# Kernel tuning notes

Hardware: AMD Instinct MI355X
Metric: run time of the kernel (lower is better)

## Reference

```python
import jax, jax.numpy as jnp
import numpy as np

UNITS = 300
MDN_MIXES = 8  # Config.mdn_mixes: 3*8=24 MDN params + 1 length = 25-dim feedback
FEAT = 25
GATE_IN = 2 * FEAT  # concat(inputs, prev_output)


def setup_inputs() -> dict:
    key = jax.random.key(0)
    ks = jax.random.split(key, 12)
    B, T = 2048, 512
    x = jax.random.uniform(ks[0], (B, T, FEAT), dtype=jnp.float32)
    s = 0.05
    kernel = jax.random.normal(ks[1], (FEAT, 4 * UNITS), dtype=jnp.float32) * s
    recurrent_kernel = jax.random.normal(ks[2], (UNITS, 4 * UNITS), dtype=jnp.float32) * s
    # unit_forget_bias: zeros except forget-gate slice = ones
    bias = jnp.concatenate([
        jnp.zeros((UNITS,), jnp.float32),
        jnp.ones((UNITS,), jnp.float32),
        jnp.zeros((2 * UNITS,), jnp.float32),
    ])
    # MLPGate: 2-layer MLP combining the two 25-dim distributions -> 24-dim
    mlp_w1 = jax.random.normal(ks[3], (GATE_IN, GATE_IN), dtype=jnp.float32) * s
    mlp_b1 = jnp.zeros((GATE_IN,), jnp.float32)
    mlp_w2 = jax.random.normal(ks[4], (GATE_IN, FEAT - 1), dtype=jnp.float32) * s
    mlp_b2 = jnp.zeros((FEAT - 1,), jnp.float32)
    # MDN heads on h (units -> mdn_mixes each)
    wa = jax.random.normal(ks[5], (UNITS, MDN_MIXES), dtype=jnp.float32) * s
    ba = jnp.zeros((MDN_MIXES,), jnp.float32)
    wm = jax.random.normal(ks[6], (UNITS, MDN_MIXES), dtype=jnp.float32) * s
    bm = jnp.zeros((MDN_MIXES,), jnp.float32)
    ws = jax.random.normal(ks[7], (UNITS, MDN_MIXES), dtype=jnp.float32) * s
    bs = jnp.zeros((MDN_MIXES,), jnp.float32)
    return {
        'x': x, 'kernel': kernel, 'recurrent_kernel': recurrent_kernel, 'bias': bias,
        'mlp_w1': mlp_w1, 'mlp_b1': mlp_b1, 'mlp_w2': mlp_w2, 'mlp_b2': mlp_b2,
        'wa': wa, 'ba': ba, 'wm': wm, 'bm': bm, 'ws': ws, 'bs': bs,
    }


def _hard_sigmoid(z):
    return jnp.clip(0.2 * z + 0.5, 0.0, 1.0)


def _nnelu(z):
    return 1.0 + jax.nn.elu(z)


def reference(x, kernel, recurrent_kernel, bias,
              mlp_w1, mlp_b1, mlp_w2, mlp_b2,
              wa, ba, wm, bm, ws, bs):
    B = x.shape[0]
    dt = x.dtype

    def step(carry, xt):
        h, c, prev = carry  # [B,U], [B,U], [B,25]
        il = xt[:, 24:25]
        pl = prev[:, 24:25]
        combined = il + pl
        denom = jnp.maximum(combined, jnp.asarray(1e-8, dt))  # LengthNormalizer
        inp2 = jnp.concatenate([xt[:, :24], il / denom], axis=1)
        prev2 = jnp.concatenate([prev[:, :24], pl / denom], axis=1)
        # MLP gate combining the two distributions
        g = jax.nn.relu(jnp.concatenate([inp2, prev2], axis=1) @ mlp_w1 + mlp_b1)
        g = g @ mlp_w2 + mlp_b2  # [B,24]
        gate_out = jnp.concatenate([g, combined], axis=1)  # [B,25]
        # LSTM gates (split-kernel math == fused without dropout)
        z = gate_out @ kernel + h @ recurrent_kernel + bias  # [B,4U]
        zi, zf, zc, zo = jnp.split(z, 4, axis=1)
        i = _hard_sigmoid(zi)
        f = _hard_sigmoid(zf)
        o = _hard_sigmoid(zo)
        c_new = f * c + i * jnp.tanh(zc)
        h_new = o * jnp.tanh(c_new)
        # MDN heads
        alpha = jax.nn.softmax(h_new @ wa + ba, axis=-1)
        mu = h_new @ wm + bm
        sigma = _nnelu(h_new @ ws + bs)
        mdn = jnp.concatenate([alpha, mu, sigma, combined], axis=1)  # [B,25]
        return (h_new, c_new, mdn), mdn

    h0 = jnp.zeros((B, UNITS), dt)
    c0 = jnp.zeros((B, UNITS), dt)
    prev0 = jnp.zeros((B, FEAT), dt)
    xt = jnp.swapaxes(x, 0, 1)  # [T,B,25]
    _, ys = jax.lax.scan(step, (h0, c0, prev0), xt)
    return jnp.swapaxes(ys, 0, 1)  # [B,T,25]
```

## Files before the change

kernel.cpp:

```cpp
#include <hip/hip_runtime.h>
#include <math.h>

#define BB 2048
#define TT 512
#define NFEAT 25
#define UNITS 300
#define RPB 16
#define NBLK (BB/RPB)
#define NT 512
#define NKS 11
#define TPW 10
#define AROW 360
#define F8ROW 352
#define GROW 72

#define OFF_B0 0
#define SZ_B0  (8*TPW*512)
#define OFF_M1 (OFF_B0 + SZ_B0)
#define SZ_M1  (4*2*512)
#define OFF_M2 (OFF_M1 + SZ_M1)
#define SZ_M2  (2*2*512)
#define OFF_H  (OFF_M2 + SZ_M2)
#define SZ_H   (2*NKS*512)
#define OFF_F8 (OFF_H + SZ_H)
#define SZ_F8B (8*100*512)
#define SW_SZ  (SZ_M1 + SZ_M2 + SZ_H)
#define SWM1   0
#define SWM2   (SZ_M1)
#define SWH    (SZ_M1 + SZ_M2)

typedef __attribute__((ext_vector_type(4))) float f32x4;
typedef __attribute__((ext_vector_type(8))) short bf16x8;

static __device__ __forceinline__ unsigned short f2bf(float f) {
    union { float f; unsigned u; } x; x.f = f;
    unsigned r = (x.u + 0x7fffu + ((x.u >> 16) & 1u)) >> 16;
    return (unsigned short)r;
}
static __device__ __forceinline__ unsigned char f2f8(float f) {
    return (unsigned char)(__builtin_amdgcn_cvt_pk_fp8_f32(f, 0.f, 0, false) & 0xff);
}
static __device__ __forceinline__ float ftanh(float v) {
    float e = __builtin_amdgcn_exp2f(v * 2.8853900817779268f);
    return 1.f - 2.f * __builtin_amdgcn_rcpf(e + 1.f);
}

static __device__ __forceinline__ int zcol(int c) { return (c & 3) * 300 + (c >> 2); }

__global__ __launch_bounds__(256) void conv_b0(
    const float* __restrict__ wk, unsigned short* __restrict__ dst)
{
    int idx = blockIdx.x * 256 + threadIdx.x;
    if (idx >= SZ_B0) return;
    int j = idx & 7, n = (idx >> 3) & 15, kg = (idx >> 7) & 3, q = idx >> 9;
    int i = q % TPW, w = q / TPW;
    int k = kg * 8 + j, c = (w + 8 * i) * 16 + n;
    float v = (k < 25 && c < 1200) ? wk[k * 1200 + zcol(c)] : 0.f;
    dst[OFF_B0 + idx] = f2bf(v);
}

__global__ __launch_bounds__(256) void conv_b8(
    const float* __restrict__ wr, unsigned char* __restrict__ dst8)
{
    int idx = blockIdx.x * 256 + threadIdx.x;
    if (idx >= SZ_F8B) return;
    int j = idx & 7, n = (idx >> 3) & 15, kg = (idx >> 7) & 3, q = idx >> 9;
    int i = q % TPW, ks1 = (q / TPW) % 10, w = q / 100;
    int k = (ks1 + 1) * 32 + kg * 8 + j, c = (w + 8 * i) * 16 + n;
    float v = (k >= 32 && k < 332 && c < 1200) ? wr[(k - 32) * 1200 + zcol(c)] : 0.f;
    dst8[idx] = f2f8(v);
}

__global__ __launch_bounds__(256) void conv_gen(
    const float* __restrict__ W, unsigned short* __restrict__ dst,
    int K, int N, int nks, int total)
{
    int idx = blockIdx.x * 256 + threadIdx.x;
    if (idx >= total) return;
    int j = idx & 7, n = (idx >> 3) & 15, kg = (idx >> 7) & 3, qq = idx >> 9;
    int ks = qq % nks, nt = qq / nks;
    int k = ks * 32 + kg * 8 + j, col = nt * 16 + n;
    float v = (k < K && col < N) ? W[k * N + col] : 0.f;
    dst[idx] = f2bf(v);
}

__global__ __launch_bounds__(256) void conv_heads(
    const float* __restrict__ wa, const float* __restrict__ wm,
    const float* __restrict__ wsg, unsigned short* __restrict__ dst)
{
    int idx = blockIdx.x * 256 + threadIdx.x;
    if (idx >= SZ_H) return;
    int j = idx & 7, n = (idx >> 3) & 15, kg = (idx >> 7) & 3, qq = idx >> 9;
    int ks = qq % NKS, nt = qq / NKS;
    int k = ks * 32 + kg * 8 + j, col = nt * 16 + n;
    float v = 0.f;
    if (k >= 32 && k < 332 && col < 24) {
        int u = k - 32, h = col >> 3, m = col & 7;
        const float* W = (h == 0) ? wa : (h == 1) ? wm : wsg;
        v = W[u * 8 + m];
    }
    dst[OFF_H + idx] = f2bf(v);
}

#define MFMA   __builtin_amdgcn_mfma_f32_16x16x32_bf16
#define MFMA8  __builtin_amdgcn_mfma_f32_16x16x32_fp8_fp8

__global__ __launch_bounds__(NT, 2)
void dilstm(
    const float* __restrict__ x,
    const unsigned short* __restrict__ wf,
    const float* __restrict__ bz,
    const float* __restrict__ b1v,
    const float* __restrict__ b2v,
    const float* __restrict__ ba,
    const float* __restrict__ bm,
    const float* __restrict__ bs,
    float* __restrict__ out)
{
    __shared__ unsigned short Abf[2][RPB][AROW];
    __shared__ __attribute__((aligned(16))) unsigned char Af8[2][RPB][F8ROW];
    __shared__ unsigned short Gbf[RPB][GROW];
    __shared__ unsigned short G1b[RPB][GROW];
    __shared__ float Sc[RPB][24];
    __shared__ float BzS[1280];
    __shared__ float B1S[64];
    __shared__ float B2S[32];
    __shared__ float Zw[8][2][16][20];
    __shared__ unsigned short SW[SW_SZ];

    const int t = threadIdx.x;
    const int lane = t & 63, wv = t >> 6;
    const int arow = lane & 15, akg = lane >> 4;
    const int crow0 = akg * 4;
    const int u_l = lane & 3, rr = lane >> 2;
    const int row0 = blockIdx.x * RPB;

    for (int i = t; i < 2 * RPB * AROW; i += NT) ((unsigned short*)Abf)[i] = 0;
    for (int i = t; i < 2 * RPB * F8ROW; i += NT) ((unsigned char*)Af8)[i] = 0;
    for (int i = t; i < RPB * GROW; i += NT) { ((unsigned short*)Gbf)[i] = 0; ((unsigned short*)G1b)[i] = 0; }
    for (int i = t; i < SW_SZ; i += NT) SW[i] = wf[OFF_M1 + i];
    for (int i = t; i < 1280; i += NT)
        BzS[i] = (i < 1200) ? bz[zcol(i)] : 0.f;
    if (t < 64) B1S[t] = (t < 50) ? b1v[t] : 0.f;
    else if (t < 96) B2S[t - 64] = (t - 64 < 24) ? b2v[t - 64] : 0.f;

    float hbias = 0.f;
    {
        int c1 = wv * 16 + arow;
        if (wv < 2 && c1 < 24)
            hbias = (c1 < 8) ? ba[c1] : (c1 < 16) ? bm[c1 - 8] : bs[c1 - 16];
    }

    float creg[TPW];
    #pragma unroll
    for (int i = 0; i < TPW; ++i) creg[i] = 0.f;

    const unsigned short* bw0 = wf + OFF_B0 + wv * (TPW * 512) + (lane << 3);
    const unsigned char*  bw8 = (const unsigned char*)(wf + OFF_F8) + (size_t)wv * (100 * 512) + (lane << 3);

    const int rA = t / 25, eA = t - (t / 25) * 25;
    float combreg = 0.f, xreg = 0.f;
    if (t < RPB * NFEAT) xreg = x[((size_t)(row0 + rA) * TT) * NFEAT + eA];
    __syncthreads();

    if (t < RPB * NFEAT) {
        if (eA < 24) {
            Gbf[rA][eA] = f2bf(xreg);
        } else {
            float comb = xreg;
            combreg = comb;
            float denom = fmaxf(comb, 1e-8f);
            Gbf[rA][24] = f2bf(xreg / denom);
            Abf[0][rA][24] = f2bf(comb);
        }
    }
    __syncthreads();

    for (int ts = 0; ts < TT; ++ts) {
        const int p = ts & 1;

        f32x4 acc[TPW];
        #pragma unroll
        for (int i = 0; i < TPW; ++i) acc[i] = (f32x4){0.f, 0.f, 0.f, 0.f};

        if (wv == 0) {
            bf16x8 ga0 = *(const bf16x8*)&Gbf[arow][akg * 8];
            bf16x8 ga1 = *(const bf16x8*)&Gbf[arow][32 + akg * 8];
            #pragma unroll
            for (int ct = 0; ct < 4; ++ct) {
                bf16x8 b0 = *(const bf16x8*)&SW[SWM1 + (ct * 2 + 0) * 512 + (lane << 3)];
                bf16x8 b1 = *(const bf16x8*)&SW[SWM1 + (ct * 2 + 1) * 512 + (lane << 3)];
                f32x4 a1c = {0.f, 0.f, 0.f, 0.f};
                a1c = MFMA(ga0, b0, a1c, 0, 0, 0);
                a1c = MFMA(ga1, b1, a1c, 0, 0, 0);
                int col = ct * 16 + arow;
                if (col < 50) {
                    #pragma unroll
                    for (int rg = 0; rg < 4; ++rg)
                        G1b[crow0 + rg][col] = f2bf(fmaxf(a1c[rg] + B1S[col], 0.f));
                }
            }
            bf16x8 ha0 = *(const bf16x8*)&G1b[arow][akg * 8];
            bf16x8 ha1 = *(const bf16x8*)&G1b[arow][32 + akg * 8];
            #pragma unroll
            for (int ct = 0; ct < 2; ++ct) {
                bf16x8 b0 = *(const bf16x8*)&SW[SWM2 + (ct * 2 + 0) * 512 + (lane << 3)];
                bf16x8 b1 = *(const bf16x8*)&SW[SWM2 + (ct * 2 + 1) * 512 + (lane << 3)];
                f32x4 a2c = {0.f, 0.f, 0.f, 0.f};
                a2c = MFMA(ha0, b0, a2c, 0, 0, 0);
                a2c = MFMA(ha1, b1, a2c, 0, 0, 0);
                int col = ct * 16 + arow;
                if (col < 24) {
                    #pragma unroll
                    for (int rg = 0; rg < 4; ++rg)
                        Abf[p][crow0 + rg][col] = f2bf(a2c[rg] + B2S[col]);
                }
            }
        }

        if (t < RPB * NFEAT && ts + 1 < TT)
            xreg = x[((size_t)(row0 + rA) * TT + (ts + 1)) * NFEAT + eA];

        {
            const unsigned char* af8p = &Af8[p][0][0] + arow * F8ROW + akg * 8;
            const unsigned char* bp = bw8;
            long long bbA[TPW], bbB[TPW];
            #pragma unroll
            for (int i = 0; i < TPW; ++i)
                bbA[i] = *(const long long*)(bp + i * 512);
            #pragma unroll 1
            for (int pr = 0; pr < 5; ++pr) {
                const int ks = 2 * pr + 1;
                #pragma unroll
                for (int i = 0; i < TPW; ++i)
                    bbB[i] = *(const long long*)(bp + 5120 + i * 512);
                long long a8a = *(const long long*)(af8p + ks * 32);
                #pragma unroll
                for (int i = 0; i < TPW; ++i)
                    acc[i] = MFMA8(a8a, bbA[i], acc[i], 0, 0, 0);
                if (pr < 4) {
                    #pragma unroll
                    for (int i = 0; i < TPW; ++i)
                        bbA[i] = *(const long long*)(bp + 10240 + i * 512);
                }
                long long a8b = *(const long long*)(af8p + ks * 32 + 32);
                #pragma unroll
                for (int i = 0; i < TPW; ++i)
                    acc[i] = MFMA8(a8b, bbB[i], acc[i], 0, 0, 0);
                bp += 10240;
            }
        }
        __syncthreads();

        {
            bf16x8 bb0[TPW];
            #pragma unroll
            for (int i = 0; i < TPW; ++i)
                bb0[i] = *(const bf16x8*)(bw0 + i * 512);
            bf16x8 aA = *(const bf16x8*)&Abf[p][arow][akg * 8];
            #pragma unroll
            for (int i = 0; i < TPW; ++i)
                acc[i] = MFMA(aA, bb0[i], acc[i], 0, 0, 0);

            *(f32x4*)&Zw[wv][0][arow][crow0] = acc[0];
            #pragma unroll
            for (int i = 0; i < TPW; ++i) {
                if (i + 1 < TPW)
                    *(f32x4*)&Zw[wv][(i + 1) & 1][arow][crow0] = acc[i + 1];
                f32x4 bz4 = *(const f32x4*)&BzS[(wv + 8 * i) * 16 + 4 * u_l];
                const float* zp = &Zw[wv][i & 1][4 * u_l][rr];
                float zi = zp[0]  + bz4[0];
                float zf = zp[20] + bz4[1];
                float zc = zp[40] + bz4[2];
                float zo = zp[60] + bz4[3];
                if (wv + 8 * i < 75) {
                    float ig = fminf(fmaxf(0.2f * zi + 0.5f, 0.f), 1.f);
                    float fg = fminf(fmaxf(0.2f * zf + 0.5f, 0.f), 1.f);
                    float og = fminf(fmaxf(0.2f * zo + 0.5f, 0.f), 1.f);
                    float cn = fg * creg[i] + ig * ftanh(zc);
                    creg[i] = cn;
                    float hn = og * ftanh(cn);
                    int hc = 32 + (wv + 8 * i) * 4 + u_l;
                    Abf[p ^ 1][rr][hc] = f2bf(hn);
                    Af8[p ^ 1][rr][hc] = f2f8(hn);
                }
            }
        }
        __syncthreads();

        if (wv < 2) {
            f32x4 acc3 = {0.f, 0.f, 0.f, 0.f};
            #pragma unroll
            for (int ks = 1; ks < NKS; ++ks) {
                bf16x8 a = *(const bf16x8*)&Abf[p ^ 1][arow][ks * 32 + akg * 8];
                bf16x8 b = *(const bf16x8*)&SW[SWH + (wv * NKS + ks) * 512 + (lane << 3)];
                acc3 = MFMA(a, b, acc3, 0, 0, 0);
            }
            int col = wv * 16 + arow;
            if (col < 24) {
                #pragma unroll
                for (int rg = 0; rg < 4; ++rg)
                    Sc[crow0 + rg][col] = acc3[rg] + hbias;
            }
        }
        __syncthreads();

        if (t < RPB * NFEAT) {
            float v;
            if (eA < 8) {
                float mx = Sc[rA][0];
                #pragma unroll
                for (int m = 1; m < 8; ++m) mx = fmaxf(mx, Sc[rA][m]);
                float sum = 0.f;
                #pragma unroll
                for (int m = 0; m < 8; ++m)
                    sum += __builtin_amdgcn_exp2f((Sc[rA][m] - mx) * 1.4426950408889634f);
                v = __builtin_amdgcn_exp2f((Sc[rA][eA] - mx) * 1.4426950408889634f) / sum;
            } else if (eA < 16) {
                v = Sc[rA][eA];
            } else if (eA < 24) {
                float s = Sc[rA][eA];
                v = (s > 0.f) ? (1.f + s) : __builtin_amdgcn_exp2f(s * 1.4426950408889634f);
            } else {
                v = combreg;
            }
            out[((size_t)(row0 + rA) * TT + ts) * NFEAT + eA] = v;
            if (eA < 24) {
                Gbf[rA][eA]      = f2bf(xreg);
                Gbf[rA][25 + eA] = f2bf(v);
            } else {
                float comb = xreg + combreg;
                float denom = fmaxf(comb, 1e-8f);
                Gbf[rA][24] = f2bf(xreg / denom);
                Gbf[rA][49] = f2bf(combreg / denom);
                Abf[p ^ 1][rA][24] = f2bf(comb);
                combreg = comb;
            }
        }
        __syncthreads();
    }
}

extern "C" void kernel_launch(void* const* d_in, const int* in_sizes, int n_in,
                              void* d_out, int out_size, void* d_ws, size_t ws_size,
                              hipStream_t stream) {
    const float* x   = (const float*)d_in[0];
    const float* wk  = (const float*)d_in[1];
    const float* wr  = (const float*)d_in[2];
    const float* bz  = (const float*)d_in[3];
    const float* w1  = (const float*)d_in[4];
    const float* b1  = (const float*)d_in[5];
    const float* w2  = (const float*)d_in[6];
    const float* b2  = (const float*)d_in[7];
    const float* wa  = (const float*)d_in[8];
    const float* ba  = (const float*)d_in[9];
    const float* wm  = (const float*)d_in[10];
    const float* bm  = (const float*)d_in[11];
    const float* wsg = (const float*)d_in[12];
    const float* bs  = (const float*)d_in[13];
    float* out = (float*)d_out;
    unsigned short* wf = (unsigned short*)d_ws;
    unsigned char*  wf8 = (unsigned char*)(wf + OFF_F8);

    conv_b0<<<(SZ_B0 + 255) / 256, 256, 0, stream>>>(wk, wf);
    conv_b8<<<(SZ_F8B + 255) / 256, 256, 0, stream>>>(wr, wf8);
    conv_gen<<<(SZ_M1 + 255) / 256, 256, 0, stream>>>(w1, wf + OFF_M1, 50, 50, 2, SZ_M1);
    conv_gen<<<(SZ_M2 + 255) / 256, 256, 0, stream>>>(w2, wf + OFF_M2, 50, 24, 2, SZ_M2);
    conv_heads<<<(SZ_H + 255) / 256, 256, 0, stream>>>(wa, wm, wsg, wf);
    dilstm<<<NBLK, NT, 0, stream>>>(x, wf, bz, b1, b2, ba, bm, bs, out);
}
```

Before: 4.139 ms.

## Fold MLP second layer into LSTM input kernel and drop double-buffered A tiles

Precomputes w2 @ kernel[:24] as a fused fp8 weight block, so the MLP's second layer and the input-kernel bf16 MFMA collapse into two extra fp8 k-slices of the recurrent GEMM. The combined-length column becomes a scalar times a row of kernel, added in fp32, and b2 is folded into the bias. The first MLP layer is spread over 4 waves instead of 1. The Abf/Af8 tiles are no longer double-buffered. This shortens the serial per-step chain and removes a bf16 GEMM pass, at the cost of fp8 precision on the fused weights and the MLP activations (scaled by 0.125 to fit the fp8 range).

```diff
diff --git a/kernel.cpp b/kernel.cpp
--- a/kernel.cpp
+++ b/kernel.cpp
@@ -8,29 +8,28 @@
 #define RPB 16
 #define NBLK (BB/RPB)
 #define NT 512
+#define KS12 12
 #define NKS 11
 #define TPW 10
-#define AROW 360
-#define F8ROW 352
+#define HROW 360
+#define F8ROW 392
 #define GROW 72
 
-#define OFF_B0 0
-#define SZ_B0  (8*TPW*512)
-#define OFF_M1 (OFF_B0 + SZ_B0)
+#define OFF_M1 0
 #define SZ_M1  (4*2*512)
-#define OFF_M2 (OFF_M1 + SZ_M1)
-#define SZ_M2  (2*2*512)
-#define OFF_H  (OFF_M2 + SZ_M2)
+#define OFF_H  (OFF_M1 + SZ_M1)
 #define SZ_H   (2*NKS*512)
-#define OFF_F8 (OFF_H + SZ_H)
-#define SZ_F8B (8*100*512)
-#define SW_SZ  (SZ_M1 + SZ_M2 + SZ_H)
+#define OFF_BZ (OFF_H + SZ_H)
+#define OFF_WK (OFF_BZ + 2560)
+#define OFF_F8 (OFF_WK + 2560)
+#define SZ_F8B (8*KS12*TPW*512)
+#define SW_SZ  (SZ_M1 + SZ_H)
 #define SWM1   0
-#define SWM2   (SZ_M1)
-#define SWH    (SZ_M1 + SZ_M2)
+#define SWH    (SZ_M1)
 
 typedef __attribute__((ext_vector_type(4))) float f32x4;
 typedef __attribute__((ext_vector_type(8))) short bf16x8;
+typedef long long ll8;
 
 static __device__ __forceinline__ unsigned short f2bf(float f) {
     union { float f; unsigned u; } x; x.f = f;
@@ -44,31 +43,51 @@
     float e = __builtin_amdgcn_exp2f(v * 2.8853900817779268f);
     return 1.f - 2.f * __builtin_amdgcn_rcpf(e + 1.f);
 }
-
 static __device__ __forceinline__ int zcol(int c) { return (c & 3) * 300 + (c >> 2); }
 
-__global__ __launch_bounds__(256) void conv_b0(
-    const float* __restrict__ wk, unsigned short* __restrict__ dst)
-{
-    int idx = blockIdx.x * 256 + threadIdx.x;
-    if (idx >= SZ_B0) return;
-    int j = idx & 7, n = (idx >> 3) & 15, kg = (idx >> 7) & 3, q = idx >> 9;
-    int i = q % TPW, w = q / TPW;
-    int k = kg * 8 + j, c = (w + 8 * i) * 16 + n;
-    float v = (k < 25 && c < 1200) ? wk[k * 1200 + zcol(c)] : 0.f;
-    dst[OFF_B0 + idx] = f2bf(v);
-}
-
 __global__ __launch_bounds__(256) void conv_b8(
-    const float* __restrict__ wr, unsigned char* __restrict__ dst8)
+    const float* __restrict__ wk, const float* __restrict__ wr,
+    const float* __restrict__ w2, unsigned char* __restrict__ dst8)
 {
     int idx = blockIdx.x * 256 + threadIdx.x;
     if (idx >= SZ_F8B) return;
     int j = idx & 7, n = (idx >> 3) & 15, kg = (idx >> 7) & 3, q = idx >> 9;
-    int i = q % TPW, ks1 = (q / TPW) % 10, w = q / 100;
-    int k = (ks1 + 1) * 32 + kg * 8 + j, c = (w + 8 * i) * 16 + n;
-    float v = (k >= 32 && k < 332 && c < 1200) ? wr[(k - 32) * 1200 + zcol(c)] : 0.f;
+    int i = q % TPW, ks = (q / TPW) % KS12, w = q / (TPW * KS12);
+    int k = ks * 32 + kg * 8 + j, c = (w + 8 * i) * 16 + n;
+    float v = 0.f;
+    if (c < 1200) {
+        int oc = zcol(c);
+        if (ks < 2) {
+            if (k < 50) {
+                float s = 0.f;
+                for (int j2 = 0; j2 < 24; ++j2)
+                    s += w2[k * 24 + j2] * wk[j2 * 1200 + oc];
+                v = 8.f * s;
+            }
+        } else {
+            int u = k - 64;
+            if (u < 300) v = wr[u * 1200 + oc];
+        }
+    }
     dst8[idx] = f2f8(v);
+}
+
+__global__ __launch_bounds__(256) void conv_misc(
+    const float* __restrict__ wk, const float* __restrict__ bz,
+    const float* __restrict__ b2, float* __restrict__ bzdst,
+    float* __restrict__ wkdst)
+{
+    int i = blockIdx.x * 256 + threadIdx.x;
+    if (i >= 1280) return;
+    float vb = 0.f, vw = 0.f;
+    if (i < 1200) {
+        int oc = zcol(i);
+        vb = bz[oc];
+        for (int j = 0; j < 24; ++j) vb += b2[j] * wk[j * 1200 + oc];
+        vw = wk[24 * 1200 + oc];
+    }
+    bzdst[i] = vb;
+    wkdst[i] = vw;
 }
 
 __global__ __launch_bounds__(256) void conv_gen(
@@ -99,7 +118,7 @@
         const float* W = (h == 0) ? wa : (h == 1) ? wm : wsg;
         v = W[u * 8 + m];
     }
-    dst[OFF_H + idx] = f2bf(v);
+    dst[idx] = f2bf(v);
 }
 
 #define MFMA   __builtin_amdgcn_mfma_f32_16x16x32_bf16
@@ -109,22 +128,21 @@
 void dilstm(
     const float* __restrict__ x,
     const unsigned short* __restrict__ wf,
-    const float* __restrict__ bz,
     const float* __restrict__ b1v,
-    const float* __restrict__ b2v,
     const float* __restrict__ ba,
     const float* __restrict__ bm,
     const float* __restrict__ bs,
     float* __restrict__ out)
 {
-    __shared__ unsigned short Abf[2][RPB][AROW];
-    __shared__ __attribute__((aligned(16))) unsigned char Af8[2][RPB][F8ROW];
+    __shared__ unsigned short Hbf[RPB][HROW];
+    __shared__ __attribute__((aligned(16))) unsigned char Af8[RPB][F8ROW];
+    __shared__ __attribute__((aligned(16))) unsigned char G1b8[RPB][64];
     __shared__ unsigned short Gbf[RPB][GROW];
-    __shared__ unsigned short G1b[RPB][GROW];
     __shared__ float Sc[RPB][24];
     __shared__ float BzS[1280];
+    __shared__ float WkS[1280];
+    __shared__ float CombS[RPB];
     __shared__ float B1S[64];
-    __shared__ float B2S[32];
     __shared__ float Zw[8][2][16][20];
     __shared__ unsigned short SW[SW_SZ];
 
@@ -135,14 +153,17 @@
     const int u_l = lane & 3, rr = lane >> 2;
     const int row0 = blockIdx.x * RPB;
 
-    for (int i = t; i < 2 * RPB * AROW; i += NT) ((unsigned short*)Abf)[i] = 0;
-    for (int i = t; i < 2 * RPB * F8ROW; i += NT) ((unsigned char*)Af8)[i] = 0;
-    for (int i = t; i < RPB * GROW; i += NT) { ((unsigned short*)Gbf)[i] = 0; ((unsigned short*)G1b)[i] = 0; }
+    for (int i = t; i < RPB * HROW; i += NT) ((unsigned short*)Hbf)[i] = 0;
+    for (int i = t; i < RPB * F8ROW; i += NT) ((unsigned char*)Af8)[i] = 0;
+    for (int i = t; i < RPB * 64; i += NT) ((unsigned char*)G1b8)[i] = 0;
+    for (int i = t; i < RPB * GROW; i += NT) ((unsigned short*)Gbf)[i] = 0;
     for (int i = t; i < SW_SZ; i += NT) SW[i] = wf[OFF_M1 + i];
-    for (int i = t; i < 1280; i += NT)
-        BzS[i] = (i < 1200) ? bz[zcol(i)] : 0.f;
+    {
+        const float* bzp = (const float*)(wf + OFF_BZ);
+        const float* wkp = (const float*)(wf + OFF_WK);
+        for (int i = t; i < 1280; i += NT) { BzS[i] = bzp[i]; WkS[i] = wkp[i]; }
+    }
     if (t < 64) B1S[t] = (t < 50) ? b1v[t] : 0.f;
-    else if (t < 96) B2S[t - 64] = (t - 64 < 24) ? b2v[t - 64] : 0.f;
 
     float hbias = 0.f;
     {
@@ -155,8 +176,9 @@
     #pragma unroll
     for (int i = 0; i < TPW; ++i) creg[i] = 0.f;
 
-    const unsigned short* bw0 = wf + OFF_B0 + wv * (TPW * 512) + (lane << 3);
-    const unsigned char*  bw8 = (const unsigned char*)(wf + OFF_F8) + (size_t)wv * (100 * 512) + (lane << 3);
+    const unsigned char* bw8 = (const unsigned char*)(wf + OFF_F8)
+                               + (size_t)wv * (KS12 * TPW * 512) + (lane << 3);
+    const unsigned char* af8p = &Af8[0][0] + arow * F8ROW + akg * 8;
 
     const int rA = t / 25, eA = t - (t / 25) * 25;
     float combreg = 0.f, xreg = 0.f;
@@ -171,50 +193,29 @@
             combreg = comb;
             float denom = fmaxf(comb, 1e-8f);
             Gbf[rA][24] = f2bf(xreg / denom);
-            Abf[0][rA][24] = f2bf(comb);
+            CombS[rA] = comb;
         }
     }
     __syncthreads();
 
     for (int ts = 0; ts < TT; ++ts) {
-        const int p = ts & 1;
-
         f32x4 acc[TPW];
         #pragma unroll
         for (int i = 0; i < TPW; ++i) acc[i] = (f32x4){0.f, 0.f, 0.f, 0.f};
 
-        if (wv == 0) {
+        if (wv < 4) {
             bf16x8 ga0 = *(const bf16x8*)&Gbf[arow][akg * 8];
             bf16x8 ga1 = *(const bf16x8*)&Gbf[arow][32 + akg * 8];
-            #pragma unroll
-            for (int ct = 0; ct < 4; ++ct) {
-                bf16x8 b0 = *(const bf16x8*)&SW[SWM1 + (ct * 2 + 0) * 512 + (lane << 3)];
-                bf16x8 b1 = *(const bf16x8*)&SW[SWM1 + (ct * 2 + 1) * 512 + (lane << 3)];
-                f32x4 a1c = {0.f, 0.f, 0.f, 0.f};
-                a1c = MFMA(ga0, b0, a1c, 0, 0, 0);
-                a1c = MFMA(ga1, b1, a1c, 0, 0, 0);
-                int col = ct * 16 + arow;
-                if (col < 50) {
-                    #pragma unroll
-                    for (int rg = 0; rg < 4; ++rg)
-                        G1b[crow0 + rg][col] = f2bf(fmaxf(a1c[rg] + B1S[col], 0.f));
-                }
-            }
-            bf16x8 ha0 = *(const bf16x8*)&G1b[arow][akg * 8];
-            bf16x8 ha1 = *(const bf16x8*)&G1b[arow][32 + akg * 8];
-            #pragma unroll
-            for (int ct = 0; ct < 2; ++ct) {
-                bf16x8 b0 = *(const bf16x8*)&SW[SWM2 + (ct * 2 + 0) * 512 + (lane << 3)];
-                bf16x8 b1 = *(const bf16x8*)&SW[SWM2 + (ct * 2 + 1) * 512 + (lane << 3)];
-                f32x4 a2c = {0.f, 0.f, 0.f, 0.f};
-                a2c = MFMA(ha0, b0, a2c, 0, 0, 0);
-                a2c = MFMA(ha1, b1, a2c, 0, 0, 0);
-                int col = ct * 16 + arow;
-                if (col < 24) {
-                    #pragma unroll
-                    for (int rg = 0; rg < 4; ++rg)
-                        Abf[p][crow0 + rg][col] = f2bf(a2c[rg] + B2S[col]);
-                }
+            bf16x8 b0 = *(const bf16x8*)&SW[SWM1 + (wv * 2 + 0) * 512 + (lane << 3)];
+            bf16x8 b1 = *(const bf16x8*)&SW[SWM1 + (wv * 2 + 1) * 512 + (lane << 3)];
+            f32x4 m1 = {0.f, 0.f, 0.f, 0.f};
+            m1 = MFMA(ga0, b0, m1, 0, 0, 0);
+            m1 = MFMA(ga1, b1, m1, 0, 0, 0);
+            int col = wv * 16 + arow;
+            if (col < 50) {
+                #pragma unroll
+                for (int rg = 0; rg < 4; ++rg)
+                    G1b8[crow0 + rg][col] = f2f8(0.125f * fmaxf(m1[rg] + B1S[col], 0.f));
             }
         }
 
@@ -222,28 +223,27 @@
             xreg = x[((size_t)(row0 + rA) * TT + (ts + 1)) * NFEAT + eA];
 
         {
-            const unsigned char* af8p = &Af8[p][0][0] + arow * F8ROW + akg * 8;
-            const unsigned char* bp = bw8;
-            long long bbA[TPW], bbB[TPW];
+            const unsigned char* bp = bw8 + 2 * (TPW * 512);
+            ll8 bbA[TPW], bbB[TPW];
             #pragma unroll
             for (int i = 0; i < TPW; ++i)
-                bbA[i] = *(const long long*)(bp + i * 512);
+                bbA[i] = *(const ll8*)(bp + i * 512);
             #pragma unroll 1
             for (int pr = 0; pr < 5; ++pr) {
-                const int ks = 2 * pr + 1;
+                const int ks = 2 * pr + 2;
                 #pragma unroll
                 for (int i = 0; i < TPW; ++i)
-                    bbB[i] = *(const long long*)(bp + 5120 + i * 512);
-                long long a8a = *(const long long*)(af8p + ks * 32);
+                    bbB[i] = *(const ll8*)(bp + 5120 + i * 512);
+                ll8 a8a = *(const ll8*)(af8p + ks * 32);
                 #pragma unroll
                 for (int i = 0; i < TPW; ++i)
                     acc[i] = MFMA8(a8a, bbA[i], acc[i], 0, 0, 0);
                 if (pr < 4) {
                     #pragma unroll
                     for (int i = 0; i < TPW; ++i)
-                        bbA[i] = *(const long long*)(bp + 10240 + i * 512);
+                        bbA[i] = *(const ll8*)(bp + 10240 + i * 512);
                 }
-                long long a8b = *(const long long*)(af8p + ks * 32 + 32);
+                ll8 a8b = *(const ll8*)(af8p + ks * 32 + 32);
                 #pragma unroll
                 for (int i = 0; i < TPW; ++i)
                     acc[i] = MFMA8(a8b, bbB[i], acc[i], 0, 0, 0);
@@ -253,26 +253,31 @@
         __syncthreads();
 
         {
-            bf16x8 bb0[TPW];
-            #pragma unroll
-            for (int i = 0; i < TPW; ++i)
-                bb0[i] = *(const bf16x8*)(bw0 + i * 512);
-            bf16x8 aA = *(const bf16x8*)&Abf[p][arow][akg * 8];
-            #pragma unroll
-            for (int i = 0; i < TPW; ++i)
-                acc[i] = MFMA(aA, bb0[i], acc[i], 0, 0, 0);
-
+            ll8 g0 = *(const ll8*)&G1b8[arow][akg * 8];
+            ll8 g1 = *(const ll8*)&G1b8[arow][32 + akg * 8];
+            ll8 c0[TPW], c1[TPW];
+            #pragma unroll
+            for (int i = 0; i < TPW; ++i) c0[i] = *(const ll8*)(bw8 + i * 512);
+            #pragma unroll
+            for (int i = 0; i < TPW; ++i) c1[i] = *(const ll8*)(bw8 + 5120 + i * 512);
+            #pragma unroll
+            for (int i = 0; i < TPW; ++i) acc[i] = MFMA8(g0, c0[i], acc[i], 0, 0, 0);
+            #pragma unroll
+            for (int i = 0; i < TPW; ++i) acc[i] = MFMA8(g1, c1[i], acc[i], 0, 0, 0);
+
+            float cmb = CombS[rr];
             *(f32x4*)&Zw[wv][0][arow][crow0] = acc[0];
             #pragma unroll
             for (int i = 0; i < TPW; ++i) {
                 if (i + 1 < TPW)
                     *(f32x4*)&Zw[wv][(i + 1) & 1][arow][crow0] = acc[i + 1];
                 f32x4 bz4 = *(const f32x4*)&BzS[(wv + 8 * i) * 16 + 4 * u_l];
+                f32x4 wk4 = *(const f32x4*)&WkS[(wv + 8 * i) * 16 + 4 * u_l];
                 const float* zp = &Zw[wv][i & 1][4 * u_l][rr];
-                float zi = zp[0]  + bz4[0];
-                float zf = zp[20] + bz4[1];
-                float zc = zp[40] + bz4[2];
-                float zo = zp[60] + bz4[3];
+                float zi = zp[0]  + bz4[0] + cmb * wk4[0];
+                float zf = zp[20] + bz4[1] + cmb * wk4[1];
+                float zc = zp[40] + bz4[2] + cmb * wk4[2];
+                float zo = zp[60] + bz4[3] + cmb * wk4[3];
                 if (wv + 8 * i < 75) {
                     float ig = fminf(fmaxf(0.2f * zi + 0.5f, 0.f), 1.f);
                     float fg = fminf(fmaxf(0.2f * zf + 0.5f, 0.f), 1.f);
@@ -280,27 +285,30 @@
                     float cn = fg * creg[i] + ig * ftanh(zc);
                     creg[i] = cn;
                     float hn = og * ftanh(cn);
-                    int hc = 32 + (wv + 8 * i) * 4 + u_l;
-                    Abf[p ^ 1][rr][hc] = f2bf(hn);
-                    Af8[p ^ 1][rr][hc] = f2f8(hn);
+                    int hb = (wv + 8 * i) * 4 + u_l;
+                    Hbf[rr][32 + hb] = f2bf(hn);
+                    Af8[rr][64 + hb] = f2f8(hn);
                 }
             }
         }
         __syncthreads();
 
         if (wv < 2) {
-            f32x4 acc3 = {0.f, 0.f, 0.f, 0.f};
-            #pragma unroll
-            for (int ks = 1; ks < NKS; ++ks) {
-                bf16x8 a = *(const bf16x8*)&Abf[p ^ 1][arow][ks * 32 + akg * 8];
-                bf16x8 b = *(const bf16x8*)&SW[SWH + (wv * NKS + ks) * 512 + (lane << 3)];
-                acc3 = MFMA(a, b, acc3, 0, 0, 0);
+            f32x4 e0 = {0.f, 0.f, 0.f, 0.f}, e1 = {0.f, 0.f, 0.f, 0.f};
+            #pragma unroll
+            for (int ks = 1; ks < NKS; ks += 2) {
+                bf16x8 a0 = *(const bf16x8*)&Hbf[arow][ks * 32 + akg * 8];
+                bf16x8 b0 = *(const bf16x8*)&SW[SWH + (wv * NKS + ks) * 512 + (lane << 3)];
+                e0 = MFMA(a0, b0, e0, 0, 0, 0);
+                bf16x8 a1 = *(const bf16x8*)&Hbf[arow][(ks + 1) * 32 + akg * 8];
+                bf16x8 b1 = *(const bf16x8*)&SW[SWH + (wv * NKS + ks + 1) * 512 + (lane << 3)];
+                e1 = MFMA(a1, b1, e1, 0, 0, 0);
             }
             int col = wv * 16 + arow;
             if (col < 24) {
                 #pragma unroll
                 for (int rg = 0; rg < 4; ++rg)
-                    Sc[crow0 + rg][col] = acc3[rg] + hbias;
+                    Sc[crow0 + rg][col] = e0[rg] + e1[rg] + hbias;
             }
         }
         __syncthreads();
@@ -333,7 +341,7 @@
                 float denom = fmaxf(comb, 1e-8f);
                 Gbf[rA][24] = f2bf(xreg / denom);
                 Gbf[rA][49] = f2bf(combreg / denom);
-                Abf[p ^ 1][rA][24] = f2bf(comb);
+                CombS[rA] = comb;
                 combreg = comb;
             }
         }
@@ -361,11 +369,12 @@
     float* out = (float*)d_out;
     unsigned short* wf = (unsigned short*)d_ws;
     unsigned char*  wf8 = (unsigned char*)(wf + OFF_F8);
-
-    conv_b0<<<(SZ_B0 + 255) / 256, 256, 0, stream>>>(wk, wf);
-    conv_b8<<<(SZ_F8B + 255) / 256, 256, 0, stream>>>(wr, wf8);
+    float* bzdst = (float*)(wf + OFF_BZ);
+    float* wkdst = (float*)(wf + OFF_WK);
+
+    conv_b8<<<(SZ_F8B + 255) / 256, 256, 0, stream>>>(wk, wr, w2, wf8);
+    conv_misc<<<(1280 + 255) / 256, 256, 0, stream>>>(wk, bz, b2, bzdst, wkdst);
     conv_gen<<<(SZ_M1 + 255) / 256, 256, 0, stream>>>(w1, wf + OFF_M1, 50, 50, 2, SZ_M1);
-    conv_gen<<<(SZ_M2 + 255) / 256, 256, 0, stream>>>(w2, wf + OFF_M2, 50, 24, 2, SZ_M2);
-    conv_heads<<<(SZ_H + 255) / 256, 256, 0, stream>>>(wa, wm, wsg, wf);
-    dilstm<<<NBLK, NT, 0, stream>>>(x, wf, bz, b1, b2, ba, bm, bs, out);
-}
+    conv_heads<<<(SZ_H + 255) / 256, 256, 0, stream>>>(wa, wm, wsg, wf + OFF_H);
+    dilstm<<<NBLK, NT, 0, stream>>>(x, wf, b1, ba, bm, bs, out);
+}
```

After: 4.320 ms. +4.4%, slower.
